# Performance work log

Hardware: AMD Instinct MI355X
Metric: run time of the kernel (lower is better)

Reference implementation:

```python
import jax, jax.numpy as jnp
import numpy as np

RADIUS = 4
NUM_LEVELS = 4
STRIDES = (1, 1, 1, 1)


def _level_corr(f1, f2, coords, r, stride):
    """Windowed bilinear correlation at one pyramid level.
    f1: [B,C,H,W] (full-res features), f2: [B,C,H2,W2] (level features),
    coords: [B,2,H,W] (x,y) already scaled to f2's resolution.
    Returns [B,(2r+1)^2,H,W].
    """
    B, C, H, W = f1.shape
    H2, W2 = f2.shape[2], f2.shape[3]
    f1t = jnp.transpose(f1, (0, 2, 3, 1))                     # [B,H,W,C]
    f2f = jnp.transpose(f2, (0, 2, 3, 1)).reshape(B, H2 * W2, C)
    d = jnp.arange(-r, r + 1, dtype=f1.dtype) * stride
    dy, dx = jnp.meshgrid(d, d, indexing='ij')
    deltas = jnp.stack([dx.ravel(), dy.ravel()], axis=-1)      # [(2r+1)^2, 2]

    def one_offset(delta):
        x = coords[:, 0] + delta[0]                            # [B,H,W]
        y = coords[:, 1] + delta[1]
        x0 = jnp.floor(x)
        y0 = jnp.floor(y)
        acc = jnp.zeros((B, H, W), f1.dtype)
        # 4 bilinear corners, zero padding outside the feature map
        for cx in (0.0, 1.0):
            for cy in (0.0, 1.0):
                xc = x0 + cx
                yc = y0 + cy
                w = (1.0 - jnp.abs(x - xc)) * (1.0 - jnp.abs(y - yc))
                valid = (xc >= 0) & (xc <= W2 - 1) & (yc >= 0) & (yc <= H2 - 1)
                idx = (jnp.clip(yc, 0, H2 - 1) * W2 + jnp.clip(xc, 0, W2 - 1)).astype(jnp.int32)
                g = jax.vmap(lambda t, i: t[i])(f2f, idx.reshape(B, -1)).reshape(B, H, W, C)
                acc = acc + jnp.where(valid, w, 0.0) * jnp.einsum('bhwc,bhwc->bhw', f1t, g)
        return acc                                             # [B,H,W]

    corr = jax.lax.map(one_offset, deltas)                     # [K,B,H,W]
    return jnp.transpose(corr, (1, 0, 2, 3))                   # [B,K,H,W]


def _corr_block(fmap1, fmap2s, coords):
    C = fmap1.shape[1]
    outs = []
    for i, f2 in enumerate(fmap2s):
        outs.append(_level_corr(fmap1, f2, coords / (2.0 ** i), RADIUS, STRIDES[i]))
    corr = jnp.concatenate(outs, axis=1)                       # [B, L*(2r+1)^2, H, W]
    return corr / jnp.sqrt(jnp.asarray(C, fmap1.dtype))


def setup_inputs() -> dict:
    key = jax.random.key(0)
    ks = jax.random.split(key, 6)
    B, C, H, W = 2, 256, 64, 64
    inp = {'fmap1': jax.random.normal(ks[0], (B, C, H, W), jnp.float32)}
    for i in range(NUM_LEVELS):
        h, w = H >> i, W >> i
        inp['fmap2_%d' % i] = jax.random.normal(ks[1 + i], (B, C, h, w), jnp.float32)
    gy, gx = jnp.meshgrid(jnp.arange(H, dtype=jnp.float32), jnp.arange(W, dtype=jnp.float32), indexing='ij')
    base = jnp.broadcast_to(jnp.stack([gx, gy], 0)[None], (B, 2, H, W))
    flow = 2.0 * jax.random.normal(jax.random.fold_in(key, 99), (B, 2, H, W), jnp.float32)
    inp['coords'] = base + flow
    return inp


def reference(fmap1, fmap2_0, fmap2_1, fmap2_2, fmap2_3, coords):
    return _corr_block(fmap1, [fmap2_0, fmap2_1, fmap2_2, fmap2_3], coords)
```

## Files before the change

### kernel.cpp

```cpp
#include <hip/hip_runtime.h>

#define RADIUS 4
#define KK 81
#define HWP 4096

typedef _Float16 f16x8 __attribute__((ext_vector_type(8)));
typedef _Float16 f16x4 __attribute__((ext_vector_type(4)));
typedef float    f32x4 __attribute__((ext_vector_type(4)));

#define OFF_F1T  0u
#define OFF_L0   4194304u
#define OFF_L1   8388608u
#define OFF_L2   9437184u
#define OFF_L3   9699328u
#define OFF_ZPAD 9764864u
#define OFF_END  9765376u

__global__ __launch_bounds__(256) void stage_kernel(
    const float* __restrict__ f1, const float* __restrict__ l0,
    const float* __restrict__ l1, const float* __restrict__ l2,
    const float* __restrict__ l3, char* __restrict__ wsB)
{
    __shared__ float tile[32][36];
    const int bx = blockIdx.x;
    const int b  = blockIdx.z;
    const int r0 = blockIdx.y * 32;
    const int t  = threadIdx.x;
    if (bx == 0 && blockIdx.y == 0 && b == 0 && t < 128)
        ((float*)(wsB + OFF_ZPAD))[t] = 0.0f;
    const float* src; _Float16* dst; int S, s0i;
    if (bx < 128)      { src = f1; dst = (_Float16*)(wsB + OFF_F1T); S = 4096; s0i = bx; }
    else if (bx < 256) { src = l0; dst = (_Float16*)(wsB + OFF_L0);  S = 4096; s0i = bx - 128; }
    else if (bx < 288) { src = l1; dst = (_Float16*)(wsB + OFF_L1);  S = 1024; s0i = bx - 256; }
    else if (bx < 296) { src = l2; dst = (_Float16*)(wsB + OFF_L2);  S = 256;  s0i = bx - 288; }
    else               { src = l3; dst = (_Float16*)(wsB + OFF_L3);  S = 64;   s0i = bx - 296; }
    const int s0 = s0i * 32;
    src += (size_t)b * 256 * S;
    dst += (size_t)b * S * 256;
    {
        const int row = t >> 3, cg = t & 7;
        *(f32x4*)&tile[row][cg * 4] =
            *(const f32x4*)&src[(size_t)(r0 + row) * S + s0 + cg * 4];
    }
    __syncthreads();
    {
        const int sidx = t >> 3, chg = t & 7;
        f16x4 o;
        o[0] = (_Float16)tile[chg * 4 + 0][sidx];
        o[1] = (_Float16)tile[chg * 4 + 1][sidx];
        o[2] = (_Float16)tile[chg * 4 + 2][sidx];
        o[3] = (_Float16)tile[chg * 4 + 3][sidx];
        *(f16x4*)&dst[(size_t)(s0 + sidx) * 256 + r0 + chg * 4] = o;
    }
}

#define BARRIER_LW { asm volatile("s_waitcnt lgkmcnt(0)" ::: "memory"); \
                     __builtin_amdgcn_s_barrier(); \
                     __builtin_amdgcn_sched_barrier(0); }

__global__ __launch_bounds__(256, 3) void corr_mfma_kernel(
    const char* __restrict__ wsB,
    const float* __restrict__ coords,
    float* __restrict__ out)
{
    __shared__ f32x4 sB[2][1024];
    __shared__ float sD[32][104];
    __shared__ int   sIx[32], sIy[32];
    __shared__ float sW[32][4];
    __shared__ int   sBox[5];

    char* sBb = (char*)sB;

    const int bx   = blockIdx.x;
    const int lvl  = blockIdx.y;
    const int tile = ((bx & 7) << 5) | (bx >> 3);
    const int b    = tile >> 7;
    const int t7   = tile & 127;
    const int tr4  = (t7 >> 3) << 2;
    const int tc8  = (t7 & 7) << 3;
    const int t    = threadIdx.x;
    const int l    = t & 63;
    const int wid  = t >> 6;
    const int aset = wid & 1;
    const int half = wid >> 1;

    const int sh = 6 - lvl;
    const int W2 = 1 << sh;

    for (int i = t; i < 32 * 104; i += 256)
        ((float*)sD)[i] = 0.0f;

    if (t < 32) {
        const int hwc = ((tr4 + (t >> 3)) << 6) + tc8 + (t & 7);
        const float sc = 1.0f / (float)(1 << lvl);
        const float xs = coords[((size_t)b * 2 + 0) * HWP + hwc] * sc;
        const float ys = coords[((size_t)b * 2 + 1) * HWP + hwc] * sc;
        const float x0f = floorf(xs), y0f = floorf(ys);
        sIx[t] = (int)x0f; sIy[t] = (int)y0f;
        const float fx = xs - x0f, fy = ys - y0f;
        sW[t][0] = (1.f - fx) * (1.f - fy);
        sW[t][1] = fx * (1.f - fy);
        sW[t][2] = (1.f - fx) * fy;
        sW[t][3] = fx * fy;
    }
    BARRIER_LW;
    if (t == 0) {
        int rlo = 1 << 20, rhi = -(1 << 20), clo = 1 << 20, chi = -(1 << 20);
        for (int px = 0; px < 32; ++px) {
            rlo = min(rlo, sIy[px]); rhi = max(rhi, sIy[px]);
            clo = min(clo, sIx[px]); chi = max(chi, sIx[px]);
        }
        const int rl = max(rlo - RADIUS, 0);
        const int rh = min(rhi + RADIUS + 1, W2 - 1);
        const int cf = max(clo - RADIUS, 0);
        const int ce = min(chi + RADIUS + 1, W2 - 1);
        const int nr = rh - rl + 1;
        const int nt = (ce >= cf) ? ((ce - cf + 16) >> 4) : 0;
        sBox[0] = rl;
        sBox[1] = cf;
        sBox[2] = nt;
        sBox[3] = (nr > 0) ? nr * nt : 0;
        sBox[4] = 65535 / max(nt, 1) + 1;
    }

    const int pxl = (aset << 4) + (l & 15);
    const int hwA = ((tr4 + (pxl >> 3)) << 6) + tc8 + (pxl & 7);
    const char* ap = wsB + OFF_F1T + ((size_t)(b * HWP + hwA)) * 512 + ((l >> 4) << 4);
    const f16x8 a0 = __builtin_bit_cast(f16x8, *(const f32x4*)(ap));
    const f16x8 a1 = __builtin_bit_cast(f16x8, *(const f32x4*)(ap + 64));
    const f16x8 a2 = __builtin_bit_cast(f16x8, *(const f32x4*)(ap + 128));
    const f16x8 a3 = __builtin_bit_cast(f16x8, *(const f32x4*)(ap + 192));
    const f16x8 a4 = __builtin_bit_cast(f16x8, *(const f32x4*)(ap + 256));
    const f16x8 a5 = __builtin_bit_cast(f16x8, *(const f32x4*)(ap + 320));
    const f16x8 a6 = __builtin_bit_cast(f16x8, *(const f32x4*)(ap + 384));
    const f16x8 a7 = __builtin_bit_cast(f16x8, *(const f32x4*)(ap + 448));
    BARRIER_LW;

    const int rlo = sBox[0], cfi = sBox[1], ntw = sBox[2];
    const int ntot = sBox[3], inv = sBox[4];
    const int NP = (ntot + 1) >> 1;
    const unsigned lvbase = ((lvl == 0) ? OFF_L0 : (lvl == 1) ? OFF_L1
                           : (lvl == 2) ? OFF_L2 : OFF_L3)
                          + (((unsigned)b << (2 * sh)) << 9);
    const int coff = l & 15;

    const int pxg  = (aset << 4) + ((l >> 4) << 2);
    const int iy0r = sIy[pxg + 0], ix0r = sIx[pxg + 0];
    const int iy1r = sIy[pxg + 1], ix1r = sIx[pxg + 1];
    const int iy2r = sIy[pxg + 2], ix2r = sIx[pxg + 2];
    const int iy3r = sIy[pxg + 3], ix3r = sIx[pxg + 3];

#define LOADP(P_, R0_, R1_, R2_, R3_) { \
        const int u_ = ((P_) << 1) + (t >> 7); \
        const unsigned q_ = ((unsigned)(u_ * inv)) >> 16; \
        const int j_ = u_ - (int)q_ * ntw; \
        const int col_ = cfi + (j_ << 4) + (t & 15); \
        const bool ok_ = (u_ < ntot) && ((unsigned)col_ < (unsigned)W2); \
        const int row_ = rlo + (int)q_; \
        const char* gp_ = wsB + (ok_ ? (lvbase + ((unsigned)((row_ << sh) + col_) << 9)) \
                                     : OFF_ZPAD) + ((unsigned)((t >> 4) & 7) << 6); \
        R0_ = *(const f32x4*)(gp_); \
        R1_ = *(const f32x4*)(gp_ + 16); \
        R2_ = *(const f32x4*)(gp_ + 32); \
        R3_ = *(const f32x4*)(gp_ + 48); \
        __builtin_amdgcn_sched_barrier(0); }

#define WRITEP(BUF_, R0_, R1_, R2_, R3_) { \
        char* wp_ = sBb + ((BUF_) << 14) + ((t >> 7) << 13) + (((t >> 4) & 7) << 10) \
                  + ((t & 15) << 4); \
        *(f32x4*)(wp_)       = R0_; \
        *(f32x4*)(wp_ + 256) = R1_; \
        *(f32x4*)(wp_ + 512) = R2_; \
        *(f32x4*)(wp_ + 768) = R3_; }

#define CONSUMEP(BUF_, P_) { \
        const int u_ = ((P_) << 1) + half; \
        if (u_ < ntot) { \
            const unsigned q_ = ((unsigned)(u_ * inv)) >> 16; \
            const int j_ = u_ - (int)q_ * ntw; \
            const int row_ = rlo + (int)q_; \
            const char* lb_ = sBb + ((BUF_) << 14) + (half << 13) + ((l >> 4) << 8) \
                            + ((l & 15) << 4); \
            const f16x8 b0_ = __builtin_bit_cast(f16x8, *(const f32x4*)(lb_)); \
            const f16x8 b1_ = __builtin_bit_cast(f16x8, *(const f32x4*)(lb_ + 1024)); \
            const f16x8 b2_ = __builtin_bit_cast(f16x8, *(const f32x4*)(lb_ + 2048)); \
            const f16x8 b3_ = __builtin_bit_cast(f16x8, *(const f32x4*)(lb_ + 3072)); \
            const f16x8 b4_ = __builtin_bit_cast(f16x8, *(const f32x4*)(lb_ + 4096)); \
            const f16x8 b5_ = __builtin_bit_cast(f16x8, *(const f32x4*)(lb_ + 5120)); \
            const f16x8 b6_ = __builtin_bit_cast(f16x8, *(const f32x4*)(lb_ + 6144)); \
            const f16x8 b7_ = __builtin_bit_cast(f16x8, *(const f32x4*)(lb_ + 7168)); \
            f32x4 ac0 = {0.f, 0.f, 0.f, 0.f}; \
            f32x4 ac1 = {0.f, 0.f, 0.f, 0.f}; \
            ac0 = __builtin_amdgcn_mfma_f32_16x16x32_f16(a0, b0_, ac0, 0, 0, 0); \
            ac1 = __builtin_amdgcn_mfma_f32_16x16x32_f16(a1, b1_, ac1, 0, 0, 0); \
            ac0 = __builtin_amdgcn_mfma_f32_16x16x32_f16(a2, b2_, ac0, 0, 0, 0); \
            ac1 = __builtin_amdgcn_mfma_f32_16x16x32_f16(a3, b3_, ac1, 0, 0, 0); \
            ac0 = __builtin_amdgcn_mfma_f32_16x16x32_f16(a4, b4_, ac0, 0, 0, 0); \
            ac1 = __builtin_amdgcn_mfma_f32_16x16x32_f16(a5, b5_, ac1, 0, 0, 0); \
            ac0 = __builtin_amdgcn_mfma_f32_16x16x32_f16(a6, b6_, ac0, 0, 0, 0); \
            ac1 = __builtin_amdgcn_mfma_f32_16x16x32_f16(a7, b7_, ac1, 0, 0, 0); \
            const f32x4 accs = ac0 + ac1; \
            const int col_ = cfi + (j_ << 4) + coff; \
            const int p0 = row_ - iy0r + RADIUS, q0 = col_ - ix0r + RADIUS; \
            if ((unsigned)p0 < 10u && (unsigned)q0 < 10u) sD[pxg + 0][p0 * 10 + q0] = accs[0]; \
            const int p1 = row_ - iy1r + RADIUS, q1 = col_ - ix1r + RADIUS; \
            if ((unsigned)p1 < 10u && (unsigned)q1 < 10u) sD[pxg + 1][p1 * 10 + q1] = accs[1]; \
            const int p2 = row_ - iy2r + RADIUS, q2 = col_ - ix2r + RADIUS; \
            if ((unsigned)p2 < 10u && (unsigned)q2 < 10u) sD[pxg + 2][p2 * 10 + q2] = accs[2]; \
            const int p3 = row_ - iy3r + RADIUS, q3 = col_ - ix3r + RADIUS; \
            if ((unsigned)p3 < 10u && (unsigned)q3 < 10u) sD[pxg + 3][p3 * 10 + q3] = accs[3]; \
        } }

    {
        f32x4 XA, XB, XC, XD, YA, YB, YC, YD;
        if (ntot > 0) {
            LOADP(0, XA, XB, XC, XD);
            if (NP > 1) LOADP(1, YA, YB, YC, YD);
            WRITEP(0, XA, XB, XC, XD);
        }
        BARRIER_LW;
        if (ntot > 0) {
            int p = 0;
            for (;;) {
                if (p + 2 < NP) LOADP(p + 2, XA, XB, XC, XD);
                CONSUMEP(p & 1, p);
                if (p + 1 < NP) WRITEP((p + 1) & 1, YA, YB, YC, YD);
                BARRIER_LW;
                if (++p >= NP) break;
                if (p + 2 < NP) LOADP(p + 2, YA, YB, YC, YD);
                CONSUMEP(p & 1, p);
                if (p + 1 < NP) WRITEP((p + 1) & 1, XA, XB, XC, XD);
                BARRIER_LW;
                if (++p >= NP) break;
            }
        }
    }
#undef LOADP
#undef WRITEP
#undef CONSUMEP
    BARRIER_LW;

    for (int j = t; j < 32 * KK; j += 256) {
        const int px = j & 31;
        const int k  = j >> 5;
        const int p  = (k * 57) >> 9;
        const int q  = k - p * 9;
        const int bi = p * 10 + q;
        const float* dd = sD[px];
        const float v = (sW[px][0] * dd[bi]      + sW[px][1] * dd[bi + 1] +
                         sW[px][2] * dd[bi + 10] + sW[px][3] * dd[bi + 11]) * 0.0625f;
        const int hwp = ((tr4 + (px >> 3)) << 6) + tc8 + (px & 7);
        out[((size_t)b * 324 + lvl * KK + k) * HWP + hwp] = v;
    }
}

__global__ __launch_bounds__(128) void corr_level_kernel(
    const float* __restrict__ f1, const float* __restrict__ f2,
    const float* __restrict__ coords, float* __restrict__ out,
    int H2, int W2, float scale, int lvl)
{
    __shared__ float sf1[256];
    __shared__ float sDl[100];
    const int pix = blockIdx.x;
    const int b   = pix >> 12;
    const int hw  = pix & 4095;
    const int t   = threadIdx.x;
    for (int c = t; c < 256; c += 128)
        sf1[c] = f1[((size_t)b * 256 + c) * 4096 + hw];
    __syncthreads();
    const float xs = coords[((size_t)b * 2 + 0) * 4096 + hw] * scale;
    const float ys = coords[((size_t)b * 2 + 1) * 4096 + hw] * scale;
    const float x0f = floorf(xs), y0f = floorf(ys);
    const float fx = xs - x0f, fy = ys - y0f;
    const int ix0 = (int)x0f, iy0 = (int)y0f;
    if (t < 100) {
        const int p = t / 10, q = t - p * 10;
        const int row = iy0 - 4 + p, col = ix0 - 4 + q;
        float acc = 0.0f;
        if (row >= 0 && row < H2 && col >= 0 && col < W2) {
            const size_t step = (size_t)H2 * W2;
            const size_t base = (size_t)b * 256 * step + (size_t)row * W2 + col;
            #pragma unroll 4
            for (int c = 0; c < 256; ++c)
                acc += f2[base + (size_t)c * step] * sf1[c];
        }
        sDl[t] = acc;
    }
    __syncthreads();
    if (t < 81) {
        const int p = t / 9, q = t - p * 9;
        const float d00 = sDl[p * 10 + q];
        const float d01 = sDl[p * 10 + q + 1];
        const float d10 = sDl[p * 10 + q + 10];
        const float d11 = sDl[p * 10 + q + 11];
        const float v = (1.0f - fy) * ((1.0f - fx) * d00 + fx * d01)
                      + fy * ((1.0f - fx) * d10 + fx * d11);
        out[((size_t)b * 324 + (size_t)lvl * 81 + t) * 4096 + hw] = v * 0.0625f;
    }
}

extern "C" void kernel_launch(void* const* d_in, const int* in_sizes, int n_in,
                              void* d_out, int out_size, void* d_ws, size_t ws_size,
                              hipStream_t stream) {
    (void)out_size;
    const float* f1     = (const float*)d_in[0];
    const float* f2l[4] = {(const float*)d_in[1], (const float*)d_in[2],
                           (const float*)d_in[3], (const float*)d_in[4]};
    const float* coords = (const float*)d_in[5];

    {
        int nbig = 0;
        for (int i = 0; i < n_in; ++i) {
            const int sz = in_sizes[i];
            if (sz == 2097152) {
                if (nbig == 0) f1 = (const float*)d_in[i];
                else           f2l[0] = (const float*)d_in[i];
                ++nbig;
            }
            else if (sz == 524288) f2l[1] = (const float*)d_in[i];
            else if (sz == 131072) f2l[2] = (const float*)d_in[i];
            else if (sz ==  32768) f2l[3] = (const float*)d_in[i];
            else if (sz ==  16384) coords = (const float*)d_in[i];
        }
    }
    float* out = (float*)d_out;
    char*  wsB = (char*)d_ws;

    if (ws_size >= (size_t)OFF_END) {
        stage_kernel<<<dim3(298, 8, 2), dim3(256, 1, 1), 0, stream>>>(
            f1, f2l[0], f2l[1], f2l[2], f2l[3], wsB);
        corr_mfma_kernel<<<dim3(256, 4, 1), 256, 0, stream>>>(wsB, coords, out);
    } else {
        for (int lvl = 0; lvl < 4; ++lvl) {
            const int W2 = 64 >> lvl;
            const float scale = 1.0f / (float)(1 << lvl);
            corr_level_kernel<<<8192, 128, 0, stream>>>(
                f1, f2l[lvl], coords, out, W2, W2, scale, lvl);
        }
    }
}
```

Baseline: 44.92 us.

## Enlarge pixel tile to 64, swizzle LDS layout and interleave level scheduling

Each block now handles an 8x8 pixel tile (64 pixels) instead of 4x8, so every wave holds its own 16-pixel A fragment and all four waves consume both staged B tiles. Each f2 window is then loaded once per 64 pixels rather than per 32, which cuts redundant global and LDS traffic. The change also adds an XOR-swizzled LDS layout to avoid bank conflicts, packs per-pixel offsets into registers, and uses a flattened 1D grid that mixes levels across XCDs in an alternating order for load balance. The costs are a larger bounding box per tile (more wasted MFMA work on out-of-window columns), more LDS, occupancy hint lowered to 2 blocks, and half as many blocks.

```diff
diff --git a/kernel.cpp b/kernel.cpp
--- a/kernel.cpp
+++ b/kernel.cpp
@@ -58,40 +58,42 @@
                      __builtin_amdgcn_s_barrier(); \
                      __builtin_amdgcn_sched_barrier(0); }
 
-__global__ __launch_bounds__(256, 3) void corr_mfma_kernel(
+__global__ __launch_bounds__(256, 2) void corr_mfma_kernel(
     const char* __restrict__ wsB,
     const float* __restrict__ coords,
     float* __restrict__ out)
 {
     __shared__ f32x4 sB[2][1024];
-    __shared__ float sD[32][104];
-    __shared__ int   sIx[32], sIy[32];
-    __shared__ float sW[32][4];
+    __shared__ float sD[64][104];
+    __shared__ int   sIx[64], sIy[64];
+    __shared__ float sW[64][4];
     __shared__ int   sBox[5];
 
     char* sBb = (char*)sB;
 
-    const int bx   = blockIdx.x;
-    const int lvl  = blockIdx.y;
-    const int tile = ((bx & 7) << 5) | (bx >> 3);
-    const int b    = tile >> 7;
-    const int t7   = tile & 127;
-    const int tr4  = (t7 >> 3) << 2;
-    const int tc8  = (t7 & 7) << 3;
+    const int id   = blockIdx.x;
+    const int gq   = id >> 3;
+    const int xcd  = id & 7;
+    const int l4   = gq & 3;
+    const int lvl  = (gq < 32) ? l4 : 3 - l4;
+    const int slot = gq >> 2;
+    const int tid  = slot * 8 + xcd;
+    const int b    = tid >> 6;
+    const int t6   = tid & 63;
+    const int tr8  = (t6 >> 3) << 3;
+    const int tc8  = (t6 & 7) << 3;
     const int t    = threadIdx.x;
     const int l    = t & 63;
     const int wid  = t >> 6;
-    const int aset = wid & 1;
-    const int half = wid >> 1;
 
     const int sh = 6 - lvl;
     const int W2 = 1 << sh;
 
-    for (int i = t; i < 32 * 104; i += 256)
+    for (int i = t; i < 64 * 104; i += 256)
         ((float*)sD)[i] = 0.0f;
 
-    if (t < 32) {
-        const int hwc = ((tr4 + (t >> 3)) << 6) + tc8 + (t & 7);
+    if (t < 64) {
+        const int hwc = ((tr8 + (t >> 3)) << 6) + tc8 + (t & 7);
         const float sc = 1.0f / (float)(1 << lvl);
         const float xs = coords[((size_t)b * 2 + 0) * HWP + hwc] * sc;
         const float ys = coords[((size_t)b * 2 + 1) * HWP + hwc] * sc;
@@ -103,10 +105,10 @@
         sW[t][2] = (1.f - fx) * fy;
         sW[t][3] = fx * fy;
     }
-    BARRIER_LW;
+    __syncthreads();
     if (t == 0) {
         int rlo = 1 << 20, rhi = -(1 << 20), clo = 1 << 20, chi = -(1 << 20);
-        for (int px = 0; px < 32; ++px) {
+        for (int px = 0; px < 64; ++px) {
             rlo = min(rlo, sIy[px]); rhi = max(rhi, sIy[px]);
             clo = min(clo, sIx[px]); chi = max(chi, sIx[px]);
         }
@@ -123,8 +125,8 @@
         sBox[4] = 65535 / max(nt, 1) + 1;
     }
 
-    const int pxl = (aset << 4) + (l & 15);
-    const int hwA = ((tr4 + (pxl >> 3)) << 6) + tc8 + (pxl & 7);
+    const int pxa = (wid << 4) + (l & 15);
+    const int hwA = ((tr8 + (pxa >> 3)) << 6) + tc8 + (pxa & 7);
     const char* ap = wsB + OFF_F1T + ((size_t)(b * HWP + hwA)) * 512 + ((l >> 4) << 4);
     const f16x8 a0 = __builtin_bit_cast(f16x8, *(const f32x4*)(ap));
     const f16x8 a1 = __builtin_bit_cast(f16x8, *(const f32x4*)(ap + 64));
@@ -134,7 +136,13 @@
     const f16x8 a5 = __builtin_bit_cast(f16x8, *(const f32x4*)(ap + 320));
     const f16x8 a6 = __builtin_bit_cast(f16x8, *(const f32x4*)(ap + 384));
     const f16x8 a7 = __builtin_bit_cast(f16x8, *(const f32x4*)(ap + 448));
-    BARRIER_LW;
+
+    const int pgl = (l >> 4) << 2;
+#define PK(J_) const int pk##J_ = ((4 - sIy[(wid << 4) + pgl + (J_)]) << 16) \
+                                | ((4 - sIx[(wid << 4) + pgl + (J_)]) & 0xffff);
+    PK(0) PK(1) PK(2) PK(3)
+#undef PK
+    __syncthreads();
 
     const int rlo = sBox[0], cfi = sBox[1], ntw = sBox[2];
     const int ntot = sBox[3], inv = sBox[4];
@@ -144,72 +152,79 @@
                           + (((unsigned)b << (2 * sh)) << 9);
     const int coff = l & 15;
 
-    const int pxg  = (aset << 4) + ((l >> 4) << 2);
-    const int iy0r = sIy[pxg + 0], ix0r = sIx[pxg + 0];
-    const int iy1r = sIy[pxg + 1], ix1r = sIx[pxg + 1];
-    const int iy2r = sIy[pxg + 2], ix2r = sIx[pxg + 2];
-    const int iy3r = sIy[pxg + 3], ix3r = sIx[pxg + 3];
+    const int scol = t >> 5;
+    const int sg   = t & 31;
+    const int wb0  = sg * 256 + ((scol ^ (sg & 7)) << 4);
+    const unsigned zpt = OFF_ZPAD + (unsigned)(sg << 4);
+    const int xor0  = (l & 7) ^ (l >> 4);
+    const int baseE = (l >> 4) * 256 + (((l & 8) | xor0) << 4);
+    const int baseO = (l >> 4) * 256 + 1024 + (((l & 8) | (xor0 ^ 4)) << 4);
+
+#define DECODE(U_, RR_, JJ_) { const unsigned q__ = ((unsigned)((U_) * inv)) >> 16; \
+        JJ_ = (U_) - (int)q__ * ntw; RR_ = rlo + (int)q__; }
 
 #define LOADP(P_, R0_, R1_, R2_, R3_) { \
-        const int u_ = ((P_) << 1) + (t >> 7); \
-        const unsigned q_ = ((unsigned)(u_ * inv)) >> 16; \
-        const int j_ = u_ - (int)q_ * ntw; \
-        const int col_ = cfi + (j_ << 4) + (t & 15); \
-        const bool ok_ = (u_ < ntot) && ((unsigned)col_ < (unsigned)W2); \
-        const int row_ = rlo + (int)q_; \
-        const char* gp_ = wsB + (ok_ ? (lvbase + ((unsigned)((row_ << sh) + col_) << 9)) \
-                                     : OFF_ZPAD) + ((unsigned)((t >> 4) & 7) << 6); \
-        R0_ = *(const f32x4*)(gp_); \
-        R1_ = *(const f32x4*)(gp_ + 16); \
-        R2_ = *(const f32x4*)(gp_ + 32); \
-        R3_ = *(const f32x4*)(gp_ + 48); \
+        { const int u_ = (P_) << 1; int r_, j_; DECODE(u_, r_, j_); \
+          const int c0_ = cfi + (j_ << 4) + scol; \
+          const unsigned rb_ = lvbase + ((unsigned)(r_ << sh) << 9) + (unsigned)(sg << 4); \
+          const char* g0_ = wsB + (((unsigned)c0_ < (unsigned)W2 && u_ < ntot) ? (rb_ + ((unsigned)c0_ << 9)) : zpt); \
+          const char* g1_ = wsB + (((unsigned)(c0_ + 8) < (unsigned)W2 && u_ < ntot) ? (rb_ + ((unsigned)(c0_ + 8) << 9)) : zpt); \
+          R0_ = *(const f32x4*)(g0_); \
+          R1_ = *(const f32x4*)(g1_); } \
+        { const int u_ = ((P_) << 1) + 1; int r_, j_; DECODE(u_, r_, j_); \
+          const int c0_ = cfi + (j_ << 4) + scol; \
+          const unsigned rb_ = lvbase + ((unsigned)(r_ << sh) << 9) + (unsigned)(sg << 4); \
+          const char* g0_ = wsB + (((unsigned)c0_ < (unsigned)W2 && u_ < ntot) ? (rb_ + ((unsigned)c0_ << 9)) : zpt); \
+          const char* g1_ = wsB + (((unsigned)(c0_ + 8) < (unsigned)W2 && u_ < ntot) ? (rb_ + ((unsigned)(c0_ + 8) << 9)) : zpt); \
+          R2_ = *(const f32x4*)(g0_); \
+          R3_ = *(const f32x4*)(g1_); } \
         __builtin_amdgcn_sched_barrier(0); }
 
 #define WRITEP(BUF_, R0_, R1_, R2_, R3_) { \
-        char* wp_ = sBb + ((BUF_) << 14) + ((t >> 7) << 13) + (((t >> 4) & 7) << 10) \
-                  + ((t & 15) << 4); \
-        *(f32x4*)(wp_)       = R0_; \
-        *(f32x4*)(wp_ + 256) = R1_; \
-        *(f32x4*)(wp_ + 512) = R2_; \
-        *(f32x4*)(wp_ + 768) = R3_; }
+        char* wp_ = sBb + ((BUF_) << 14) + wb0; \
+        *(f32x4*)(wp_)        = R0_; \
+        *(f32x4*)(wp_ + 128)  = R1_; \
+        *(f32x4*)(wp_ + 8192) = R2_; \
+        *(f32x4*)(wp_ + 8320) = R3_; }
+
+#define CONS1(BASEB_, U_) { \
+        int r_, j_; DECODE(U_, r_, j_); \
+        const char* pE_ = (BASEB_) + baseE; \
+        const char* pO_ = (BASEB_) + baseO; \
+        const f16x8 b0_ = __builtin_bit_cast(f16x8, *(const f32x4*)(pE_)); \
+        const f16x8 b1_ = __builtin_bit_cast(f16x8, *(const f32x4*)(pO_)); \
+        const f16x8 b2_ = __builtin_bit_cast(f16x8, *(const f32x4*)(pE_ + 2048)); \
+        const f16x8 b3_ = __builtin_bit_cast(f16x8, *(const f32x4*)(pO_ + 2048)); \
+        const f16x8 b4_ = __builtin_bit_cast(f16x8, *(const f32x4*)(pE_ + 4096)); \
+        const f16x8 b5_ = __builtin_bit_cast(f16x8, *(const f32x4*)(pO_ + 4096)); \
+        const f16x8 b6_ = __builtin_bit_cast(f16x8, *(const f32x4*)(pE_ + 6144)); \
+        const f16x8 b7_ = __builtin_bit_cast(f16x8, *(const f32x4*)(pO_ + 6144)); \
+        f32x4 ac0 = {0.f, 0.f, 0.f, 0.f}; \
+        f32x4 ac1 = {0.f, 0.f, 0.f, 0.f}; \
+        ac0 = __builtin_amdgcn_mfma_f32_16x16x32_f16(a0, b0_, ac0, 0, 0, 0); \
+        ac1 = __builtin_amdgcn_mfma_f32_16x16x32_f16(a1, b1_, ac1, 0, 0, 0); \
+        ac0 = __builtin_amdgcn_mfma_f32_16x16x32_f16(a2, b2_, ac0, 0, 0, 0); \
+        ac1 = __builtin_amdgcn_mfma_f32_16x16x32_f16(a3, b3_, ac1, 0, 0, 0); \
+        ac0 = __builtin_amdgcn_mfma_f32_16x16x32_f16(a4, b4_, ac0, 0, 0, 0); \
+        ac1 = __builtin_amdgcn_mfma_f32_16x16x32_f16(a5, b5_, ac1, 0, 0, 0); \
+        ac0 = __builtin_amdgcn_mfma_f32_16x16x32_f16(a6, b6_, ac0, 0, 0, 0); \
+        ac1 = __builtin_amdgcn_mfma_f32_16x16x32_f16(a7, b7_, ac1, 0, 0, 0); \
+        const f32x4 ss = ac0 + ac1; \
+        const int col_ = cfi + (j_ << 4) + coff; \
+        { const int p_ = r_ + (pk0 >> 16), q_ = col_ + ((pk0 << 16) >> 16); \
+          if ((unsigned)p_ < 10u && (unsigned)q_ < 10u) sD[(wid << 4) + pgl + 0][p_ * 10 + q_] = ss[0]; } \
+        { const int p_ = r_ + (pk1 >> 16), q_ = col_ + ((pk1 << 16) >> 16); \
+          if ((unsigned)p_ < 10u && (unsigned)q_ < 10u) sD[(wid << 4) + pgl + 1][p_ * 10 + q_] = ss[1]; } \
+        { const int p_ = r_ + (pk2 >> 16), q_ = col_ + ((pk2 << 16) >> 16); \
+          if ((unsigned)p_ < 10u && (unsigned)q_ < 10u) sD[(wid << 4) + pgl + 2][p_ * 10 + q_] = ss[2]; } \
+        { const int p_ = r_ + (pk3 >> 16), q_ = col_ + ((pk3 << 16) >> 16); \
+          if ((unsigned)p_ < 10u && (unsigned)q_ < 10u) sD[(wid << 4) + pgl + 3][p_ * 10 + q_] = ss[3]; } }
 
 #define CONSUMEP(BUF_, P_) { \
-        const int u_ = ((P_) << 1) + half; \
-        if (u_ < ntot) { \
-            const unsigned q_ = ((unsigned)(u_ * inv)) >> 16; \
-            const int j_ = u_ - (int)q_ * ntw; \
-            const int row_ = rlo + (int)q_; \
-            const char* lb_ = sBb + ((BUF_) << 14) + (half << 13) + ((l >> 4) << 8) \
-                            + ((l & 15) << 4); \
-            const f16x8 b0_ = __builtin_bit_cast(f16x8, *(const f32x4*)(lb_)); \
-            const f16x8 b1_ = __builtin_bit_cast(f16x8, *(const f32x4*)(lb_ + 1024)); \
-            const f16x8 b2_ = __builtin_bit_cast(f16x8, *(const f32x4*)(lb_ + 2048)); \
-            const f16x8 b3_ = __builtin_bit_cast(f16x8, *(const f32x4*)(lb_ + 3072)); \
-            const f16x8 b4_ = __builtin_bit_cast(f16x8, *(const f32x4*)(lb_ + 4096)); \
-            const f16x8 b5_ = __builtin_bit_cast(f16x8, *(const f32x4*)(lb_ + 5120)); \
-            const f16x8 b6_ = __builtin_bit_cast(f16x8, *(const f32x4*)(lb_ + 6144)); \
-            const f16x8 b7_ = __builtin_bit_cast(f16x8, *(const f32x4*)(lb_ + 7168)); \
-            f32x4 ac0 = {0.f, 0.f, 0.f, 0.f}; \
-            f32x4 ac1 = {0.f, 0.f, 0.f, 0.f}; \
-            ac0 = __builtin_amdgcn_mfma_f32_16x16x32_f16(a0, b0_, ac0, 0, 0, 0); \
-            ac1 = __builtin_amdgcn_mfma_f32_16x16x32_f16(a1, b1_, ac1, 0, 0, 0); \
-            ac0 = __builtin_amdgcn_mfma_f32_16x16x32_f16(a2, b2_, ac0, 0, 0, 0); \
-            ac1 = __builtin_amdgcn_mfma_f32_16x16x32_f16(a3, b3_, ac1, 0, 0, 0); \
-            ac0 = __builtin_amdgcn_mfma_f32_16x16x32_f16(a4, b4_, ac0, 0, 0, 0); \
-            ac1 = __builtin_amdgcn_mfma_f32_16x16x32_f16(a5, b5_, ac1, 0, 0, 0); \
-            ac0 = __builtin_amdgcn_mfma_f32_16x16x32_f16(a6, b6_, ac0, 0, 0, 0); \
-            ac1 = __builtin_amdgcn_mfma_f32_16x16x32_f16(a7, b7_, ac1, 0, 0, 0); \
-            const f32x4 accs = ac0 + ac1; \
-            const int col_ = cfi + (j_ << 4) + coff; \
-            const int p0 = row_ - iy0r + RADIUS, q0 = col_ - ix0r + RADIUS; \
-            if ((unsigned)p0 < 10u && (unsigned)q0 < 10u) sD[pxg + 0][p0 * 10 + q0] = accs[0]; \
-            const int p1 = row_ - iy1r + RADIUS, q1 = col_ - ix1r + RADIUS; \
-            if ((unsigned)p1 < 10u && (unsigned)q1 < 10u) sD[pxg + 1][p1 * 10 + q1] = accs[1]; \
-            const int p2 = row_ - iy2r + RADIUS, q2 = col_ - ix2r + RADIUS; \
-            if ((unsigned)p2 < 10u && (unsigned)q2 < 10u) sD[pxg + 2][p2 * 10 + q2] = accs[2]; \
-            const int p3 = row_ - iy3r + RADIUS, q3 = col_ - ix3r + RADIUS; \
-            if ((unsigned)p3 < 10u && (unsigned)q3 < 10u) sD[pxg + 3][p3 * 10 + q3] = accs[3]; \
-        } }
+        const char* bb_ = sBb + ((BUF_) << 14); \
+        const int u0_ = (P_) << 1; \
+        CONS1(bb_, u0_); \
+        if (u0_ + 1 < ntot) { CONS1(bb_ + 8192, u0_ + 1); } }
 
     {
         f32x4 XA, XB, XC, XD, YA, YB, YC, YD;
@@ -235,21 +250,23 @@
             }
         }
     }
+#undef DECODE
 #undef LOADP
 #undef WRITEP
+#undef CONS1
 #undef CONSUMEP
-    BARRIER_LW;
-
-    for (int j = t; j < 32 * KK; j += 256) {
-        const int px = j & 31;
-        const int k  = j >> 5;
+    __syncthreads();
+
+    for (int j = t; j < 64 * KK; j += 256) {
+        const int px = j & 63;
+        const int k  = j >> 6;
         const int p  = (k * 57) >> 9;
         const int q  = k - p * 9;
         const int bi = p * 10 + q;
         const float* dd = sD[px];
         const float v = (sW[px][0] * dd[bi]      + sW[px][1] * dd[bi + 1] +
                          sW[px][2] * dd[bi + 10] + sW[px][3] * dd[bi + 11]) * 0.0625f;
-        const int hwp = ((tr4 + (px >> 3)) << 6) + tc8 + (px & 7);
+        const int hwp = ((tr8 + (px >> 3)) << 6) + tc8 + (px & 7);
         out[((size_t)b * 324 + lvl * KK + k) * HWP + hwp] = v;
     }
 }
@@ -329,7 +346,7 @@
     if (ws_size >= (size_t)OFF_END) {
         stage_kernel<<<dim3(298, 8, 2), dim3(256, 1, 1), 0, stream>>>(
             f1, f2l[0], f2l[1], f2l[2], f2l[3], wsB);
-        corr_mfma_kernel<<<dim3(256, 4, 1), 256, 0, stream>>>(wsB, coords, out);
+        corr_mfma_kernel<<<dim3(512, 1, 1), 256, 0, stream>>>(wsB, coords, out);
     } else {
         for (int lvl = 0; lvl < 4; ++lvl) {
             const int W2 = 64 >> lvl;
```

Measured after the change: 47.12 us. +4.9%, slower.
